# Optimization experiments

Hardware: AMD Instinct MI355X
Metric: run time of the kernel (lower is better)

## Reference

```python
import jax, jax.numpy as jnp
import numpy as np

N, IN_DIM, MLPW, HID, NCLS = 2048, 1024, 16, 256, 4


def setup_inputs() -> dict:
    key = jax.random.key(0)
    ks = jax.random.split(key, 12)
    f32 = jnp.float32
    return {
        "x": jax.random.normal(ks[0], (N, IN_DIM), f32),
        "adj": jax.random.uniform(ks[1], (N, N), f32),
        "xdeg": jax.random.uniform(ks[2], (N, N), f32),
        "ydeg": jax.random.uniform(ks[3], (N, N), f32),
        # edge MLP([3, mlp_width, 2])
        "Wm1": jax.random.normal(ks[4], (3, MLPW), f32) * (1.0 / np.sqrt(3.0)),
        "bm1": jnp.zeros((MLPW,), f32),
        "Wm2": jax.random.normal(ks[5], (MLPW, 2), f32) * (1.0 / np.sqrt(MLPW)),
        "bm2": jnp.zeros((2,), f32),
        # GCN / dense layers (stored as [in, out]; torch Linear applies x @ W.T)
        "Wg1": jax.random.normal(ks[6], (IN_DIM, HID), f32) * (1.0 / np.sqrt(IN_DIM)),
        "Wl2": jax.random.normal(ks[7], (HID, 64), f32) * (1.0 / np.sqrt(HID)),
        "bl2": jnp.zeros((64,), f32),
        "Wg2": jax.random.normal(ks[8], (64, NCLS), f32) * (1.0 / 8.0),
    }


def reference(x, adj, xdeg, ydeg, Wm1, bm1, Wm2, bm2, Wg1, Wl2, bl2, Wg2):
    n = adj.shape[0]
    # Edge-feature MLP mask. The torch code gathers nonzero entries, runs the
    # MLP, scatters back into a zero buffer, then multiplies by adj. Computing
    # the mask densely is mathematically identical because adj * mask is zero
    # wherever adj is zero.
    feats = jnp.stack([adj, xdeg, ydeg], axis=-1)          # [N, N, 3]
    h = jax.nn.relu(feats @ Wm1 + bm1)                     # [N, N, MLPW]
    mask = jax.nn.softmax(h @ Wm2 + bm2, axis=-1)[..., 1]  # [N, N]
    A = adj * mask + jnp.eye(n, dtype=adj.dtype)
    # Symmetric-ish normalization: D_row^{-1/2} A D_col^{-1/2}
    # (the torch diag-matmul chain reduces to this row/col scaling).
    rowsum = jnp.sum(A, axis=1)
    colsum = jnp.sum(A, axis=0)
    dr = jnp.where(rowsum > 0, jax.lax.rsqrt(jnp.where(rowsum > 0, rowsum, 1.0)), 0.0)
    dc = jnp.where(colsum > 0, jax.lax.rsqrt(jnp.where(colsum > 0, colsum, 1.0)), 0.0)
    A = dr[:, None] * A * dc[None, :]
    # GCN layer 1 (dropout = identity in eval mode)
    hid = (A @ (x @ Wg1)) @ Wl2 + bl2                      # [N, 64]
    # GCN layer 2
    out = A @ (hid @ Wg2)                                  # [N, n_classes]
    return out, hid
```

## Files before the change

### kernel.cpp

```cpp
#include <hip/hip_runtime.h>

#define NN 2048
#define MLPW 16

typedef __attribute__((ext_vector_type(8))) short short8v;
typedef __attribute__((ext_vector_type(16))) float float16v;
typedef __attribute__((ext_vector_type(4))) unsigned short ushort4v;
typedef __attribute__((ext_vector_type(8))) unsigned short ushort8v;

__device__ __forceinline__ unsigned short f2b(float f) {
  unsigned int u = __float_as_uint(f);
  unsigned int r = (u + 0x7fffu + ((u >> 16) & 1u)) >> 16;
  return (unsigned short)r;
}
__device__ __forceinline__ float b2f(unsigned short u) {
  return __uint_as_float(((unsigned int)u) << 16);
}

__global__ void __launch_bounds__(256) edge_kernel(
    const float* __restrict__ adj, const float* __restrict__ xdeg,
    const float* __restrict__ ydeg,
    const float* __restrict__ Wm1, const float* __restrict__ bm1,
    const float* __restrict__ Wm2, const float* __restrict__ bm2,
    unsigned short* __restrict__ Abf, float* __restrict__ dr) {
  __shared__ float w1[48], b1[16], w2[32], b2s[2];
  __shared__ float wsum[4];
  const int tid = threadIdx.x;
  if (tid < 48) w1[tid] = Wm1[tid];
  if (tid < 16) b1[tid] = bm1[tid];
  if (tid < 32) w2[tid] = Wm2[tid];
  if (tid < 2) b2s[tid] = bm2[tid];
  __syncthreads();
  const int i = blockIdx.x;
  const float4* adj4 = (const float4*)(adj + (size_t)i * NN);
  const float4* xd4 = (const float4*)(xdeg + (size_t)i * NN);
  const float4* yd4 = (const float4*)(ydeg + (size_t)i * NN);
  ushort4v* A4 = (ushort4v*)(Abf + (size_t)i * NN);
  float rsum = 0.f;
  for (int j4 = tid; j4 < NN / 4; j4 += 256) {
    float4 av = adj4[j4], xv = xd4[j4], yv = yd4[j4];
    float aa[4] = {av.x, av.y, av.z, av.w};
    float xx[4] = {xv.x, xv.y, xv.z, xv.w};
    float yy[4] = {yv.x, yv.y, yv.z, yv.w};
    ushort4v oo;
#pragma unroll
    for (int e = 0; e < 4; e++) {
      float l0 = b2s[0], l1 = b2s[1];
#pragma unroll
      for (int k = 0; k < MLPW; k++) {
        float h = fmaf(aa[e], w1[k], fmaf(xx[e], w1[16 + k], fmaf(yy[e], w1[32 + k], b1[k])));
        h = fmaxf(h, 0.f);
        l0 = fmaf(h, w2[2 * k], l0);
        l1 = fmaf(h, w2[2 * k + 1], l1);
      }
      float mask = 1.f / (1.f + __expf(l0 - l1));
      float v = aa[e] * mask;
      int j = j4 * 4 + e;
      if (j == i) v += 1.f;
      oo[e] = f2b(v);
      rsum += v;
    }
    A4[j4] = oo;
  }
#pragma unroll
  for (int off = 32; off > 0; off >>= 1) rsum += __shfl_down(rsum, off);
  if ((tid & 63) == 0) wsum[tid >> 6] = rsum;
  __syncthreads();
  if (tid == 0) {
    float t = wsum[0] + wsum[1] + wsum[2] + wsum[3];
    dr[i] = t > 0.f ? rsqrtf(t) : 0.f;
  }
}

__global__ void __launch_bounds__(256) colsum_kernel(
    const unsigned short* __restrict__ Abf, float* __restrict__ partial) {
  const int j0 = threadIdx.x * 8;
  const int i0 = blockIdx.x * 64;
  float s[8] = {0, 0, 0, 0, 0, 0, 0, 0};
  for (int i = 0; i < 64; i++) {
    ushort8v a = *(const ushort8v*)&Abf[(size_t)(i0 + i) * NN + j0];
#pragma unroll
    for (int e = 0; e < 8; e++) s[e] += b2f(a[e]);
  }
  float* p = partial + (size_t)blockIdx.x * NN + j0;
  *(float4*)p = make_float4(s[0], s[1], s[2], s[3]);
  *(float4*)(p + 4) = make_float4(s[4], s[5], s[6], s[7]);
}

__global__ void __launch_bounds__(256) dc_kernel(
    const float* __restrict__ partial, float* __restrict__ dc) {
  const int j = blockIdx.x * 256 + threadIdx.x;
  float s = 0.f;
#pragma unroll
  for (int p = 0; p < 32; p++) s += partial[(size_t)p * NN + j];
  dc[j] = s > 0.f ? rsqrtf(s) : 0.f;
}

template <bool A_F32T, bool B_F32>
__global__ void __launch_bounds__(256) gemm_splitk_kernel(
    const void* __restrict__ Av, const void* __restrict__ Bv,
    float* __restrict__ P, int M, int N, int K, int Kc, int lda) {
  constexpr int SW = 136;
  __shared__ unsigned short As[32 * SW];
  __shared__ unsigned short Bs[128 * SW];
  const int tid = threadIdx.x;
  const int lane = tid & 63, wave = tid >> 6;
  const int l31 = lane & 31, half = lane >> 5;
  const int row0 = blockIdx.y * 32, col0 = blockIdx.x * 128;
  const int kbeg = blockIdx.z * Kc;

  float16v acc;
#pragma unroll
  for (int r = 0; r < 16; r++) acc[r] = 0.f;

  for (int k0 = 0; k0 < Kc; k0 += 128) {
    if (A_F32T) {
      const int kidx = tid >> 1, nh = (tid & 1) * 16;
      const float* src = (const float*)Av + (size_t)(kbeg + k0 + kidx) * lda + row0 + nh;
      float4 v0 = ((const float4*)src)[0], v1 = ((const float4*)src)[1];
      float4 v2 = ((const float4*)src)[2], v3 = ((const float4*)src)[3];
      const float vv[16] = {v0.x, v0.y, v0.z, v0.w, v1.x, v1.y, v1.z, v1.w,
                            v2.x, v2.y, v2.z, v2.w, v3.x, v3.y, v3.z, v3.w};
#pragma unroll
      for (int e = 0; e < 16; e++) As[(nh + e) * SW + kidx] = f2b(vv[e]);
    } else {
      const unsigned short* Ab = (const unsigned short*)Av;
#pragma unroll
      for (int i = 0; i < 2; i++) {
        const int id = tid + i * 256;
        const int r = id >> 4, c = id & 15;
        *(ushort8v*)&As[r * SW + c * 8] =
            *(const ushort8v*)&Ab[(size_t)(row0 + r) * K + kbeg + k0 + c * 8];
      }
    }
#pragma unroll
    for (int i = 0; i < 8; i++) {
      const int id = tid + i * 256;
      const int r = id >> 4, c = id & 15;
      if (B_F32) {
        const float* bp = (const float*)Bv + (size_t)(col0 + r) * K + kbeg + k0 + c * 8;
        float4 u = *(const float4*)bp, v = *(const float4*)(bp + 4);
        ushort8v pk = {f2b(u.x), f2b(u.y), f2b(u.z), f2b(u.w),
                       f2b(v.x), f2b(v.y), f2b(v.z), f2b(v.w)};
        *(ushort8v*)&Bs[r * SW + c * 8] = pk;
      } else {
        *(ushort8v*)&Bs[r * SW + c * 8] =
            *(const ushort8v*)&((const unsigned short*)Bv)[(size_t)(col0 + r) * K + kbeg + k0 + c * 8];
      }
    }
    __syncthreads();
#pragma unroll
    for (int ks = 0; ks < 8; ks++) {
      short8v a = *(const short8v*)&As[l31 * SW + ks * 16 + half * 8];
      short8v b = *(const short8v*)&Bs[(wave * 32 + l31) * SW + ks * 16 + half * 8];
      acc = __builtin_amdgcn_mfma_f32_32x32x16_bf16(a, b, acc, 0, 0, 0);
    }
    __syncthreads();
  }
  float* Pb = P + ((size_t)blockIdx.z * M + row0) * N + col0 + wave * 32 + l31;
#pragma unroll
  for (int reg = 0; reg < 16; reg++) {
    const int m = (reg & 3) + 8 * (reg >> 2) + 4 * half;
    Pb[(size_t)m * N] = acc[reg];
  }
}

__global__ void __launch_bounds__(256) reduce_xwt_kernel(
    const float* __restrict__ P, const float* __restrict__ dc,
    unsigned short* __restrict__ XWT) {
  const int t = blockIdx.x * 256 + threadIdx.x;
  const int i = t >> 8;
  const int j0 = (t & 255) * 8;
  float s[8] = {0, 0, 0, 0, 0, 0, 0, 0};
#pragma unroll
  for (int sk = 0; sk < 4; sk++) {
    const float* p = P + ((size_t)sk * 256 + i) * 2048 + j0;
    float4 u = *(const float4*)p, v = *(const float4*)(p + 4);
    s[0] += u.x; s[1] += u.y; s[2] += u.z; s[3] += u.w;
    s[4] += v.x; s[5] += v.y; s[6] += v.z; s[7] += v.w;
  }
  float4 d0 = *(const float4*)&dc[j0], d1 = *(const float4*)&dc[j0 + 4];
  ushort8v o = {f2b(s[0] * d0.x), f2b(s[1] * d0.y), f2b(s[2] * d0.z), f2b(s[3] * d0.w),
                f2b(s[4] * d1.x), f2b(s[5] * d1.y), f2b(s[6] * d1.z), f2b(s[7] * d1.w)};
  *(ushort8v*)&XWT[(size_t)i * 2048 + j0] = o;
}

__global__ void __launch_bounds__(256) tail_kernel(
    const float* __restrict__ P2, const float* __restrict__ dr,
    const float* __restrict__ dc, const float* __restrict__ Wl2,
    const float* __restrict__ bl2, const float* __restrict__ Wg2,
    float* __restrict__ hid, float* __restrict__ HW) {
  __shared__ float T1s[16][256];
  __shared__ float hidS[16][68];
  const int m0 = blockIdx.x * 16;
  const int tid = threadIdx.x;
#pragma unroll
  for (int i = 0; i < 16; i++) {
    const int idx = tid + i * 256;
    const int mi = idx >> 8, n = idx & 255;
    float s = 0.f;
#pragma unroll
    for (int sk = 0; sk < 4; sk++)
      s += P2[((size_t)sk * 2048 + m0 + mi) * 256 + n];
    T1s[mi][n] = s * dr[m0 + mi];
  }
  __syncthreads();
  const int j = tid & 63, mg = tid >> 6;
  float h[4] = {bl2[j], bl2[j], bl2[j], bl2[j]};
  for (int n = 0; n < 256; n++) {
    float w = Wl2[(size_t)n * 64 + j];
#pragma unroll
    for (int r = 0; r < 4; r++) h[r] = fmaf(T1s[mg * 4 + r][n], w, h[r]);
  }
#pragma unroll
  for (int r = 0; r < 4; r++) {
    hid[(size_t)(m0 + mg * 4 + r) * 64 + j] = h[r];
    hidS[mg * 4 + r][j] = h[r];
  }
  __syncthreads();
  if (tid < 64) {
    const int r = tid >> 2, c = tid & 3;
    float s = 0.f;
#pragma unroll
    for (int jj = 0; jj < 64; jj++) s = fmaf(hidS[r][jj], Wg2[jj * 4 + c], s);
    HW[(size_t)(m0 + r) * 4 + c] = s * dc[m0 + r];
  }
}

__global__ void __launch_bounds__(256) out_kernel(
    const unsigned short* __restrict__ Abf, const float* __restrict__ HW,
    const float* __restrict__ dr, float* __restrict__ outp) {
  const int i = blockIdx.x, tid = threadIdx.x;
  const ushort8v a8 = ((const ushort8v*)(Abf + (size_t)i * NN))[tid];
  const float4* hw4 = (const float4*)HW;
  const int j0 = tid * 8;
  float ax = 0.f, ay = 0.f, az = 0.f, aw = 0.f;
#pragma unroll
  for (int e = 0; e < 8; e++) {
    float a = b2f(a8[e]);
    float4 h = hw4[j0 + e];
    ax = fmaf(a, h.x, ax);
    ay = fmaf(a, h.y, ay);
    az = fmaf(a, h.z, az);
    aw = fmaf(a, h.w, aw);
  }
  __shared__ float red[4][256];
  red[0][tid] = ax; red[1][tid] = ay; red[2][tid] = az; red[3][tid] = aw;
  __syncthreads();
  for (int s = 128; s > 0; s >>= 1) {
    if (tid < s) {
      red[0][tid] += red[0][tid + s];
      red[1][tid] += red[1][tid + s];
      red[2][tid] += red[2][tid + s];
      red[3][tid] += red[3][tid + s];
    }
    __syncthreads();
  }
  if (tid < 4) outp[(size_t)i * 4 + tid] = dr[i] * red[tid][0];
}

extern "C" void kernel_launch(void* const* d_in, const int* in_sizes, int n_in,
                              void* d_out, int out_size, void* d_ws, size_t ws_size,
                              hipStream_t stream) {
  const float* x    = (const float*)d_in[0];
  const float* adj  = (const float*)d_in[1];
  const float* xdeg = (const float*)d_in[2];
  const float* ydeg = (const float*)d_in[3];
  const float* Wm1  = (const float*)d_in[4];
  const float* bm1  = (const float*)d_in[5];
  const float* Wm2  = (const float*)d_in[6];
  const float* bm2  = (const float*)d_in[7];
  const float* Wg1  = (const float*)d_in[8];
  const float* Wl2  = (const float*)d_in[9];
  const float* bl2  = (const float*)d_in[10];
  const float* Wg2  = (const float*)d_in[11];

  char* ws = (char*)d_ws;
  unsigned short* Abf  = (unsigned short*)(ws);
  unsigned short* XWT  = (unsigned short*)(ws + 8388608);
  float* P    = (float*)(ws + 9437184);
  float* part = (float*)(ws + 18350080);
  float* dr   = (float*)(ws + 18612224);
  float* dc   = (float*)(ws + 18620416);
  float* HW   = (float*)(ws + 18628608);

  float* outp = (float*)d_out;
  float* hid  = (float*)d_out + 2048 * 4;

  edge_kernel<<<NN, 256, 0, stream>>>(adj, xdeg, ydeg, Wm1, bm1, Wm2, bm2, Abf, dr);
  colsum_kernel<<<32, 256, 0, stream>>>(Abf, part);
  dc_kernel<<<NN / 256, 256, 0, stream>>>(part, dc);
  gemm_splitk_kernel<true, true><<<dim3(2048 / 128, 256 / 32, 4), 256, 0, stream>>>(
      Wg1, x, P, 256, 2048, 1024, 256, 256);
  reduce_xwt_kernel<<<256, 256, 0, stream>>>(P, dc, XWT);
  gemm_splitk_kernel<false, false><<<dim3(256 / 128, 2048 / 32, 4), 256, 0, stream>>>(
      Abf, XWT, P, 2048, 256, 2048, 512, 0);
  tail_kernel<<<2048 / 16, 256, 0, stream>>>(P, dr, dc, Wl2, bl2, Wg2, hid, HW);
  out_kernel<<<NN, 256, 0, stream>>>(Abf, HW, dr, outp);
}
```

Measured before the change: 179.3 us.

## Fuse column-sum partials into edge kernel, processing 8 rows per block

The edge-MLP kernel now handles 8 rows per block, with each thread owning 8 columns. It accumulates per-column partial sums in registers and writes them out, so the separate colsum kernel that re-read the bf16 adjacency no longer runs. dc_kernel now reduces 256 partials per column instead of 32, and the workspace offsets move to fit the larger partial buffer. Fewer blocks (256) with more work each may lower latency hiding, and the final column reduction gets longer.

```diff
diff --git a/kernel.cpp b/kernel.cpp
--- a/kernel.cpp
+++ b/kernel.cpp
@@ -22,29 +22,36 @@
     const float* __restrict__ ydeg,
     const float* __restrict__ Wm1, const float* __restrict__ bm1,
     const float* __restrict__ Wm2, const float* __restrict__ bm2,
-    unsigned short* __restrict__ Abf, float* __restrict__ dr) {
+    unsigned short* __restrict__ Abf, float* __restrict__ dr,
+    float* __restrict__ partial) {
   __shared__ float w1[48], b1[16], w2[32], b2s[2];
-  __shared__ float wsum[4];
+  __shared__ float wsum[8][4];
   const int tid = threadIdx.x;
   if (tid < 48) w1[tid] = Wm1[tid];
   if (tid < 16) b1[tid] = bm1[tid];
   if (tid < 32) w2[tid] = Wm2[tid];
   if (tid < 2) b2s[tid] = bm2[tid];
   __syncthreads();
-  const int i = blockIdx.x;
-  const float4* adj4 = (const float4*)(adj + (size_t)i * NN);
-  const float4* xd4 = (const float4*)(xdeg + (size_t)i * NN);
-  const float4* yd4 = (const float4*)(ydeg + (size_t)i * NN);
-  ushort4v* A4 = (ushort4v*)(Abf + (size_t)i * NN);
-  float rsum = 0.f;
-  for (int j4 = tid; j4 < NN / 4; j4 += 256) {
-    float4 av = adj4[j4], xv = xd4[j4], yv = yd4[j4];
-    float aa[4] = {av.x, av.y, av.z, av.w};
-    float xx[4] = {xv.x, xv.y, xv.z, xv.w};
-    float yy[4] = {yv.x, yv.y, yv.z, yv.w};
-    ushort4v oo;
-#pragma unroll
-    for (int e = 0; e < 4; e++) {
+  const int i0 = blockIdx.x * 8;
+  const int j0 = tid * 8;
+  const int lane = tid & 63, wave = tid >> 6;
+  float cacc[8] = {0, 0, 0, 0, 0, 0, 0, 0};
+#pragma unroll
+  for (int r = 0; r < 8; r++) {
+    const int i = i0 + r;
+    const float* ap = adj + (size_t)i * NN + j0;
+    const float* xp = xdeg + (size_t)i * NN + j0;
+    const float* yp = ydeg + (size_t)i * NN + j0;
+    float4 a0 = ((const float4*)ap)[0], a1 = ((const float4*)ap)[1];
+    float4 x0 = ((const float4*)xp)[0], x1 = ((const float4*)xp)[1];
+    float4 y0 = ((const float4*)yp)[0], y1 = ((const float4*)yp)[1];
+    const float aa[8] = {a0.x, a0.y, a0.z, a0.w, a1.x, a1.y, a1.z, a1.w};
+    const float xx[8] = {x0.x, x0.y, x0.z, x0.w, x1.x, x1.y, x1.z, x1.w};
+    const float yy[8] = {y0.x, y0.y, y0.z, y0.w, y1.x, y1.y, y1.z, y1.w};
+    ushort8v oo;
+    float rs = 0.f;
+#pragma unroll
+    for (int e = 0; e < 8; e++) {
       float l0 = b2s[0], l1 = b2s[1];
 #pragma unroll
       for (int k = 0; k < MLPW; k++) {
@@ -55,44 +62,32 @@
       }
       float mask = 1.f / (1.f + __expf(l0 - l1));
       float v = aa[e] * mask;
-      int j = j4 * 4 + e;
-      if (j == i) v += 1.f;
+      if (j0 + e == i) v += 1.f;
       oo[e] = f2b(v);
-      rsum += v;
-    }
-    A4[j4] = oo;
-  }
-#pragma unroll
-  for (int off = 32; off > 0; off >>= 1) rsum += __shfl_down(rsum, off);
-  if ((tid & 63) == 0) wsum[tid >> 6] = rsum;
-  __syncthreads();
-  if (tid == 0) {
-    float t = wsum[0] + wsum[1] + wsum[2] + wsum[3];
-    dr[i] = t > 0.f ? rsqrtf(t) : 0.f;
-  }
-}
-
-__global__ void __launch_bounds__(256) colsum_kernel(
-    const unsigned short* __restrict__ Abf, float* __restrict__ partial) {
-  const int j0 = threadIdx.x * 8;
-  const int i0 = blockIdx.x * 64;
-  float s[8] = {0, 0, 0, 0, 0, 0, 0, 0};
-  for (int i = 0; i < 64; i++) {
-    ushort8v a = *(const ushort8v*)&Abf[(size_t)(i0 + i) * NN + j0];
-#pragma unroll
-    for (int e = 0; e < 8; e++) s[e] += b2f(a[e]);
-  }
-  float* p = partial + (size_t)blockIdx.x * NN + j0;
-  *(float4*)p = make_float4(s[0], s[1], s[2], s[3]);
-  *(float4*)(p + 4) = make_float4(s[4], s[5], s[6], s[7]);
+      rs += v;
+      cacc[e] += v;
+    }
+    *(ushort8v*)&Abf[(size_t)i * NN + j0] = oo;
+#pragma unroll
+    for (int off = 32; off > 0; off >>= 1) rs += __shfl_down(rs, off);
+    if (lane == 0) wsum[r][wave] = rs;
+  }
+  float* pp = partial + (size_t)blockIdx.x * NN + j0;
+  *(float4*)pp = make_float4(cacc[0], cacc[1], cacc[2], cacc[3]);
+  *(float4*)(pp + 4) = make_float4(cacc[4], cacc[5], cacc[6], cacc[7]);
+  __syncthreads();
+  if (tid < 8) {
+    float t = wsum[tid][0] + wsum[tid][1] + wsum[tid][2] + wsum[tid][3];
+    dr[i0 + tid] = t > 0.f ? rsqrtf(t) : 0.f;
+  }
 }
 
 __global__ void __launch_bounds__(256) dc_kernel(
     const float* __restrict__ partial, float* __restrict__ dc) {
   const int j = blockIdx.x * 256 + threadIdx.x;
   float s = 0.f;
-#pragma unroll
-  for (int p = 0; p < 32; p++) s += partial[(size_t)p * NN + j];
+#pragma unroll 4
+  for (int p = 0; p < 256; p++) s += partial[(size_t)p * NN + j];
   dc[j] = s > 0.f ? rsqrtf(s) : 0.f;
 }
 
@@ -279,16 +274,16 @@
   unsigned short* Abf  = (unsigned short*)(ws);
   unsigned short* XWT  = (unsigned short*)(ws + 8388608);
   float* P    = (float*)(ws + 9437184);
-  float* part = (float*)(ws + 18350080);
-  float* dr   = (float*)(ws + 18612224);
-  float* dc   = (float*)(ws + 18620416);
-  float* HW   = (float*)(ws + 18628608);
+  float* part = (float*)(ws + 17825792);
+  float* dr   = (float*)(ws + 19922944);
+  float* dc   = (float*)(ws + 19931136);
+  float* HW   = (float*)(ws + 19939328);
 
   float* outp = (float*)d_out;
   float* hid  = (float*)d_out + 2048 * 4;
 
-  edge_kernel<<<NN, 256, 0, stream>>>(adj, xdeg, ydeg, Wm1, bm1, Wm2, bm2, Abf, dr);
-  colsum_kernel<<<32, 256, 0, stream>>>(Abf, part);
+  edge_kernel<<<NN / 8, 256, 0, stream>>>(adj, xdeg, ydeg, Wm1, bm1, Wm2, bm2,
+                                          Abf, dr, part);
   dc_kernel<<<NN / 256, 256, 0, stream>>>(part, dc);
   gemm_splitk_kernel<true, true><<<dim3(2048 / 128, 256 / 32, 4), 256, 0, stream>>>(
       Wg1, x, P, 256, 2048, 1024, 256, 256);
```

Result: slower. 195.1 us (+8.8%).
